# Performance work log

Measured on AMD Instinct MI355X. Metric: run time of the kernel, lower is better.

The kernel has to match this reference:

```python
import jax, jax.numpy as jnp
import numpy as np

B, S, H, E, F, TOP_K = 4, 2048, 512, 16, 1024, 2


def setup_inputs() -> dict:
    key = jax.random.key(0)
    k0, k1, k2, k3, k4 = jax.random.split(key, 5)
    scale = 0.02
    return {
        "inputs": jax.random.normal(k0, (B, S, H), dtype=jnp.float32),
        "router_w": jax.random.normal(k1, (E, H), dtype=jnp.float32) * scale,
        "gate_w": jax.random.normal(k2, (E, H, F), dtype=jnp.float32) * scale,
        "up_w": jax.random.normal(k3, (E, H, F), dtype=jnp.float32) * scale,
        "down_w": jax.random.normal(k4, (E, F, H), dtype=jnp.float32) * scale,
    }


def _moe_forward(inputs, router_w, gate_w, up_w, down_w):
    b, s, h = inputs.shape
    x = inputs.reshape(-1, h)                      # [T, H]
    T = x.shape[0]
    # --- routing: topk of logits then fp32 softmax over the k selected ---
    router_logits = x @ router_w.T                 # [T, E]
    top_vals, top_idx = jax.lax.top_k(router_logits, TOP_K)   # [T, K]
    weights = jax.nn.softmax(top_vals.astype(jnp.float32), axis=-1)  # [T, K]
    # dense combine weights: w[t, e] = routing weight if expert e selected else 0
    combine = jnp.zeros((T, router_w.shape[0]), jnp.float32)
    combine = combine.at[jnp.arange(T)[:, None], top_idx].set(weights)  # [T, E]

    # --- per-expert SwiGLU MLP, weighted combine (scan over experts) ---
    def step(acc, ew):
        wg, wu, wd, ce = ew                        # [H,F], [H,F], [F,H], [T]
        hid = jax.nn.silu(x @ wg) * (x @ wu)       # [T, F]
        y = hid @ wd                               # [T, H]
        return acc + ce[:, None] * y, None

    out0 = jnp.zeros_like(x)
    out, _ = jax.lax.scan(step, out0, (gate_w, up_w, down_w, combine.T))
    return out.reshape(b, s, h), router_logits, top_idx


def reference(inputs, router_w, gate_w, up_w, down_w):
    out, router_logits, selected_experts = _moe_forward(
        inputs, router_w, gate_w, up_w, down_w)
    return out
```

## Files before the change

kernel.cpp:

```cpp
#include <hip/hip_runtime.h>
#include <cstdint>
#include <cstddef>

#define T_TOK 8192
#define H_DIM 512
#define E_NUM 16
#define F_DIM 1024

typedef __bf16 bf16x8 __attribute__((ext_vector_type(8)));
typedef float f32x4 __attribute__((ext_vector_type(4)));

#define OFF_XBF  0UL
#define OFF_HID  8388608UL
#define OFF_GW   41943040UL
#define OFF_UW   58720256UL
#define OFF_DW   75497472UL
#define OFF_STOK 92274688UL
#define OFF_SW   92340224UL
#define OFF_TOPE 92405760UL
#define OFF_TOPW 92471296UL
#define OFF_CNT  92536832UL
#define OFF_CUR  92537856UL
#define OFF_OFFS 92538880UL

__device__ __forceinline__ unsigned short f2bf(float f) {
  union { float f; uint32_t u; } v; v.f = f;
  uint32_t r = v.u + 0x7fffu + ((v.u >> 16) & 1u);
  return (unsigned short)(r >> 16);
}

__device__ __forceinline__ void gld16(const void* g, void* l) {
  __builtin_amdgcn_global_load_lds(
      (const __attribute__((address_space(1))) unsigned int*)g,
      (__attribute__((address_space(3))) unsigned int*)l, 16, 0, 0);
}

__global__ __launch_bounds__(256) void k_pre(
    const float* __restrict__ x, const float* __restrict__ rw,
    const float* __restrict__ gw, const float* __restrict__ uw,
    const float* __restrict__ dw,
    unsigned short* __restrict__ xbf, int* __restrict__ tope,
    float* __restrict__ topw,
    unsigned short* __restrict__ gws, unsigned short* __restrict__ uws,
    unsigned short* __restrict__ dws) {
  const int bid = blockIdx.x;
  const int tid = threadIdx.x;
  __shared__ float ls[32 * 260];

  if (bid < 4096) {
    const int fx = bid & 7, kc = (bid >> 3) & 15, ez = bid >> 7;
    const int e = ez >> 1;
    const float* src = ((ez & 1) ? uw : gw) + (size_t)e * H_DIM * F_DIM;
    unsigned short* dst = ((ez & 1) ? uws : gws);
    #pragma unroll
    for (int j = 0; j < 4; ++j) {
      int vi = tid + j * 256;
      int row = vi >> 5, c4 = (vi & 31) * 4;
      float4 v = *(const float4*)&src[(size_t)(kc*32 + row) * F_DIM + fx*128 + c4];
      ls[row*132 + c4+0]=v.x; ls[row*132 + c4+1]=v.y;
      ls[row*132 + c4+2]=v.z; ls[row*132 + c4+3]=v.w;
    }
    __syncthreads();
    size_t obase = (((size_t)e * 8 + fx) * 16 + kc) * 4096;
    #pragma unroll
    for (int j = 0; j < 2; ++j) {
      int oi = tid + j * 256;
      int f = oi >> 2, slot = oi & 3;
      int ks = ((slot ^ f) & 3) * 8;
      uint4 o;
      o.x = (uint32_t)f2bf(ls[(ks+0)*132 + f]) | ((uint32_t)f2bf(ls[(ks+1)*132 + f]) << 16);
      o.y = (uint32_t)f2bf(ls[(ks+2)*132 + f]) | ((uint32_t)f2bf(ls[(ks+3)*132 + f]) << 16);
      o.z = (uint32_t)f2bf(ls[(ks+4)*132 + f]) | ((uint32_t)f2bf(ls[(ks+5)*132 + f]) << 16);
      o.w = (uint32_t)f2bf(ls[(ks+6)*132 + f]) | ((uint32_t)f2bf(ls[(ks+7)*132 + f]) << 16);
      *(uint4*)&dst[obase + (size_t)oi * 8] = o;
    }
  } else if (bid < 5120) {
    const int i = bid - 4096;
    const int ht = i & 1, kc = (i >> 1) & 31, e = i >> 6;
    const float* src = dw + (size_t)e * F_DIM * H_DIM;
    #pragma unroll
    for (int j = 0; j < 8; ++j) {
      int vi = tid + j * 256;
      int row = vi >> 6, c4 = (vi & 63) * 4;
      float4 v = *(const float4*)&src[(size_t)(kc*32 + row) * H_DIM + ht*256 + c4];
      ls[row*260 + c4+0]=v.x; ls[row*260 + c4+1]=v.y;
      ls[row*260 + c4+2]=v.z; ls[row*260 + c4+3]=v.w;
    }
    __syncthreads();
    size_t obase = (((size_t)e * 2 + ht) * 32 + kc) * 8192;
    #pragma unroll
    for (int j = 0; j < 4; ++j) {
      int oi = tid + j * 256;
      int h = oi >> 2, slot = oi & 3;
      int ks = ((slot ^ h) & 3) * 8;
      uint4 o;
      o.x = (uint32_t)f2bf(ls[(ks+0)*260 + h]) | ((uint32_t)f2bf(ls[(ks+1)*260 + h]) << 16);
      o.y = (uint32_t)f2bf(ls[(ks+2)*260 + h]) | ((uint32_t)f2bf(ls[(ks+3)*260 + h]) << 16);
      o.z = (uint32_t)f2bf(ls[(ks+4)*260 + h]) | ((uint32_t)f2bf(ls[(ks+5)*260 + h]) << 16);
      o.w = (uint32_t)f2bf(ls[(ks+6)*260 + h]) | ((uint32_t)f2bf(ls[(ks+7)*260 + h]) << 16);
      *(uint4*)&dws[obase + (size_t)oi * 8] = o;
    }
  } else {
    const int rb = bid - 5120;
    const int wave = tid >> 6, lane = tid & 63;
    const int t = rb * 4 + wave;
    const float4* xr = (const float4*)(x + (size_t)t * H_DIM + lane * 8);
    float4 a = xr[0], b = xr[1];
    float xi[8] = {a.x, a.y, a.z, a.w, b.x, b.y, b.z, b.w};
    uint4 o;
    o.x = (uint32_t)f2bf(xi[0]) | ((uint32_t)f2bf(xi[1]) << 16);
    o.y = (uint32_t)f2bf(xi[2]) | ((uint32_t)f2bf(xi[3]) << 16);
    o.z = (uint32_t)f2bf(xi[4]) | ((uint32_t)f2bf(xi[5]) << 16);
    o.w = (uint32_t)f2bf(xi[6]) | ((uint32_t)f2bf(xi[7]) << 16);
    *(uint4*)(xbf + (size_t)t * H_DIM + lane * 8) = o;
    float acc[E_NUM];
    #pragma unroll
    for (int e = 0; e < E_NUM; ++e) {
      const float4* wr = (const float4*)(rw + e * H_DIM + lane * 8);
      float4 wa = wr[0], wb = wr[1];
      acc[e] = xi[0]*wa.x + xi[1]*wa.y + xi[2]*wa.z + xi[3]*wa.w
             + xi[4]*wb.x + xi[5]*wb.y + xi[6]*wb.z + xi[7]*wb.w;
    }
    #pragma unroll
    for (int off = 1; off < 64; off <<= 1) {
      #pragma unroll
      for (int e = 0; e < E_NUM; ++e) acc[e] += __shfl_xor(acc[e], off);
    }
    if (lane == 0) {
      int e0 = 0; float v0 = acc[0];
      #pragma unroll
      for (int e = 1; e < E_NUM; ++e) if (acc[e] > v0) { v0 = acc[e]; e0 = e; }
      int e1 = -1; float v1 = -3.4e38f;
      #pragma unroll
      for (int e = 0; e < E_NUM; ++e) if (e != e0 && acc[e] > v1) { v1 = acc[e]; e1 = e; }
      float ee = __expf(v1 - v0);
      float inv = 1.0f / (1.0f + ee);
      tope[t*2]   = e0; tope[t*2+1] = e1;
      topw[t*2]   = inv; topw[t*2+1] = ee * inv;
    }
  }
}

__global__ __launch_bounds__(256) void k_hist(
    const int* __restrict__ tope, int* __restrict__ counts) {
  __shared__ int lh[E_NUM];
  const int tid = threadIdx.x;
  if (tid < E_NUM) lh[tid] = 0;
  __syncthreads();
  atomicAdd(&lh[tope[blockIdx.x * 256 + tid]], 1);
  __syncthreads();
  if (tid < E_NUM) atomicAdd(&counts[tid * 16], lh[tid]);
}

__global__ void k_offsets(const int* __restrict__ counts, int* __restrict__ offs) {
  if (threadIdx.x == 0 && blockIdx.x == 0) {
    int s = 0;
    for (int e = 0; e < E_NUM; ++e) { offs[e] = s; s += counts[e * 16]; }
    offs[E_NUM] = s;
  }
}

__global__ __launch_bounds__(256) void k_scatter(
    const int* __restrict__ tope, const float* __restrict__ topw,
    const int* __restrict__ offs, int* __restrict__ cursors,
    int* __restrict__ stok, float* __restrict__ sw) {
  __shared__ int lh[E_NUM];
  __shared__ int lbase[E_NUM];
  const int tid = threadIdx.x;
  const int t = blockIdx.x * 256 + tid;
  if (tid < E_NUM) lh[tid] = 0;
  __syncthreads();
  int e0 = tope[t*2], e1 = tope[t*2+1];
  int r0 = atomicAdd(&lh[e0], 1);
  int r1 = atomicAdd(&lh[e1], 1);
  __syncthreads();
  if (tid < E_NUM) lbase[tid] = atomicAdd(&cursors[tid * 16], lh[tid]);
  __syncthreads();
  int s0 = offs[e0] + lbase[e0] + r0;
  int s1 = offs[e1] + lbase[e1] + r1;
  stok[s0] = t; sw[s0] = topw[t*2];
  stok[s1] = t; sw[s1] = topw[t*2+1];
}

__global__ __launch_bounds__(256, 2) void k_gateup(
    const unsigned short* __restrict__ xbf,
    const unsigned short* __restrict__ gws, const unsigned short* __restrict__ uws,
    const int* __restrict__ stok, const int* __restrict__ counts,
    const int* __restrict__ offs, unsigned short* __restrict__ hid) {
  const int e = blockIdx.z;
  const int cnt = counts[e * 16];
  const int t0 = blockIdx.y * 128;
  if (t0 >= cnt) return;
  const int base = offs[e];
  const int fx = blockIdx.x;

  __shared__ __align__(16) unsigned short sb[2][3][4096];

  const int tid = threadIdx.x;
  const int wave = tid >> 6, lane = tid & 63;
  const int l15 = lane & 15, hi = lane >> 4;
  const int wm = wave >> 1, wn = wave & 1;

  const int r0 = tid >> 2, slot = tid & 3;
  const int rr0 = min(t0 + r0, cnt - 1), rr1 = min(t0 + r0 + 64, cnt - 1);
  const char* sA0 = (const char*)xbf + (size_t)stok[base + rr0] * 1024 + ((slot ^ (r0 & 3)) * 16);
  const char* sA1 = (const char*)xbf + (size_t)stok[base + rr1] * 1024 + ((slot ^ (r0 & 3)) * 16);
  const char* sG = (const char*)gws + (((size_t)e * 8 + fx) * 16) * 8192 + tid * 16;
  const char* sU = (const char*)uws + (((size_t)e * 8 + fx) * 16) * 8192 + tid * 16;
  unsigned short* const dA = &sb[0][0][wave * 512];
  unsigned short* const dG = &sb[0][1][wave * 512];
  unsigned short* const dU = &sb[0][2][wave * 512];
  const int bufo = 3 * 4096;

  f32x4 accg[4][4] = {}; f32x4 accu[4][4] = {};

  #define STAGE_GU(b, kk) { \
    gld16(sA0 + (kk)*64, dA + (b)*bufo); \
    gld16(sA1 + (kk)*64, dA + (b)*bufo + 2048); \
    gld16(sG + (size_t)(kk)*8192, dG + (b)*bufo); \
    gld16(sG + (size_t)(kk)*8192 + 4096, dG + (b)*bufo + 2048); \
    gld16(sU + (size_t)(kk)*8192, dU + (b)*bufo); \
    gld16(sU + (size_t)(kk)*8192 + 4096, dU + (b)*bufo + 2048); }

  STAGE_GU(0, 0);
  __syncthreads();
  #pragma unroll 1
  for (int kk = 0; kk < 16; ++kk) {
    const int cur = kk & 1;
    if (kk < 15) STAGE_GU(cur ^ 1, kk + 1);
    const unsigned short* lA = &sb[cur][0][0];
    const unsigned short* lG = &sb[cur][1][0];
    const unsigned short* lU = &sb[cur][2][0];
    bf16x8 a[4], bg[4], bu[4];
    #pragma unroll
    for (int m = 0; m < 4; ++m) {
      int row = wm*64 + m*16 + l15;
      a[m] = *(const bf16x8*)((const char*)lA + row*64 + (((hi ^ row) & 3) << 4));
    }
    #pragma unroll
    for (int s = 0; s < 4; ++s) {
      int row = wn*64 + s*16 + l15;
      int o = row*64 + (((hi ^ row) & 3) << 4);
      bg[s] = *(const bf16x8*)((const char*)lG + o);
      bu[s] = *(const bf16x8*)((const char*)lU + o);
    }
    #pragma unroll
    for (int m = 0; m < 4; ++m)
      #pragma unroll
      for (int s = 0; s < 4; ++s) {
        accg[m][s] = __builtin_amdgcn_mfma_f32_16x16x32_bf16(a[m], bg[s], accg[m][s], 0, 0, 0);
        accu[m][s] = __builtin_amdgcn_mfma_f32_16x16x32_bf16(a[m], bu[s], accu[m][s], 0, 0, 0);
      }
    __syncthreads();
  }
  #undef STAGE_GU

  #pragma unroll
  for (int m = 0; m < 4; ++m)
    #pragma unroll
    for (int r = 0; r < 4; ++r) {
      int row = t0 + wm*64 + m*16 + hi*4 + r;
      if (row < cnt) {
        #pragma unroll
        for (int s = 0; s < 4; ++s) {
          float g = accg[m][s][r], u = accu[m][s][r];
          float h = g / (1.0f + __expf(-g)) * u;
          hid[(size_t)(base + row) * 1024 + fx*128 + wn*64 + s*16 + l15] = f2bf(h);
        }
      }
    }
}

__global__ __launch_bounds__(256, 3) void k_down(
    const unsigned short* __restrict__ hid, const unsigned short* __restrict__ dws,
    const int* __restrict__ stok, const float* __restrict__ sw,
    const int* __restrict__ counts, const int* __restrict__ offs,
    float* __restrict__ out) {
  const int e = blockIdx.z;
  const int cnt = counts[e * 16];
  const int t0 = blockIdx.y * 64;
  if (t0 >= cnt) return;
  const int base = offs[e];
  const int ht = blockIdx.x;

  __shared__ __align__(16) unsigned short sbA[2][2048];
  __shared__ __align__(16) unsigned short sbW[2][8192];

  const int tid = threadIdx.x;
  const int wave = tid >> 6, lane = tid & 63;
  const int l15 = lane & 15, hi = lane >> 4;

  const int r0 = tid >> 2, slot = tid & 3;
  const int rr = min(t0 + r0, cnt - 1);
  const char* sA = (const char*)hid + (size_t)(base + rr) * 2048 + ((slot ^ (r0 & 3)) * 16);
  const char* sW = (const char*)dws + (((size_t)e * 2 + ht) * 32) * 16384 + tid * 16;
  unsigned short* const dA = &sbA[0][wave * 512];
  unsigned short* const dW = &sbW[0][wave * 512];

  f32x4 acc[4][4] = {};

  #define STAGE_DN(b, kk) { \
    gld16(sA + (kk)*64, dA + (b)*2048); \
    const char* w = sW + (size_t)(kk)*16384; \
    gld16(w,         dW + (b)*8192); \
    gld16(w + 4096,  dW + (b)*8192 + 2048); \
    gld16(w + 8192,  dW + (b)*8192 + 4096); \
    gld16(w + 12288, dW + (b)*8192 + 6144); }

  STAGE_DN(0, 0);
  __syncthreads();
  #pragma unroll 1
  for (int kk = 0; kk < 32; ++kk) {
    const int cur = kk & 1;
    if (kk < 31) STAGE_DN(cur ^ 1, kk + 1);
    const unsigned short* lA = &sbA[cur][0];
    const unsigned short* lW = &sbW[cur][0];
    bf16x8 a[4], b[4];
    #pragma unroll
    for (int m = 0; m < 4; ++m) {
      int row = m*16 + l15;
      a[m] = *(const bf16x8*)((const char*)lA + row*64 + (((hi ^ row) & 3) << 4));
    }
    #pragma unroll
    for (int s = 0; s < 4; ++s) {
      int row = wave*64 + s*16 + l15;
      b[s] = *(const bf16x8*)((const char*)lW + row*64 + (((hi ^ row) & 3) << 4));
    }
    #pragma unroll
    for (int m = 0; m < 4; ++m)
      #pragma unroll
      for (int s = 0; s < 4; ++s)
        acc[m][s] = __builtin_amdgcn_mfma_f32_16x16x32_bf16(a[m], b[s], acc[m][s], 0, 0, 0);
    __syncthreads();
  }
  #undef STAGE_DN

  #pragma unroll
  for (int m = 0; m < 4; ++m)
    #pragma unroll
    for (int r = 0; r < 4; ++r) {
      int row = t0 + m*16 + hi*4 + r;
      if (row < cnt) {
        int sl = base + row;
        int t = stok[sl];
        float w = sw[sl];
        float* orow = out + (size_t)t * H_DIM + ht*256 + wave*64;
        #pragma unroll
        for (int s = 0; s < 4; ++s)
          atomicAdd(&orow[s*16 + l15], w * acc[m][s][r]);
      }
    }
}

extern "C" void kernel_launch(void* const* d_in, const int* in_sizes, int n_in,
                              void* d_out, int out_size, void* d_ws, size_t ws_size,
                              hipStream_t stream) {
  const float* x  = (const float*)d_in[0];
  const float* rw = (const float*)d_in[1];
  const float* gw = (const float*)d_in[2];
  const float* uw = (const float*)d_in[3];
  const float* dw = (const float*)d_in[4];
  float* out = (float*)d_out;
  char* ws = (char*)d_ws;

  unsigned short* xbf = (unsigned short*)(ws + OFF_XBF);
  unsigned short* hid = (unsigned short*)(ws + OFF_HID);
  unsigned short* gws = (unsigned short*)(ws + OFF_GW);
  unsigned short* uws = (unsigned short*)(ws + OFF_UW);
  unsigned short* dws = (unsigned short*)(ws + OFF_DW);
  int*   stok    = (int*)(ws + OFF_STOK);
  float* swt     = (float*)(ws + OFF_SW);
  int*   tope    = (int*)(ws + OFF_TOPE);
  float* topw    = (float*)(ws + OFF_TOPW);
  int*   counts  = (int*)(ws + OFF_CNT);
  int*   cursors = (int*)(ws + OFF_CUR);
  int*   offs    = (int*)(ws + OFF_OFFS);

  hipMemsetAsync(ws + OFF_CNT, 0, 2048 + 128, stream);
  hipMemsetAsync(d_out, 0, (size_t)T_TOK * H_DIM * sizeof(float), stream);

  k_pre<<<7168, 256, 0, stream>>>(x, rw, gw, uw, dw, xbf, tope, topw, gws, uws, dws);
  k_hist<<<T_TOK * 2 / 256, 256, 0, stream>>>(tope, counts);
  k_offsets<<<1, 64, 0, stream>>>(counts, offs);
  k_scatter<<<T_TOK / 256, 256, 0, stream>>>(tope, topw, offs, cursors, stok, swt);
  k_gateup<<<dim3(8, T_TOK * 2 / 128, E_NUM), 256, 0, stream>>>(
      xbf, gws, uws, stok, counts, offs, hid);
  k_down<<<dim3(2, T_TOK * 2 / 64, E_NUM), 256, 0, stream>>>(
      hid, dws, stok, swt, counts, offs, out);
}
```

Before: 172.9 us.

## Replace atomic scatter-add combine with bf16 expert outputs and per-token gather

The down-projection kernel now writes unweighted bf16 results per sorted slot into a buffer that reuses the gate-weight workspace region, instead of doing weighted fp32 atomicAdds into the output. A new gather kernel reads each token's two slot rows via a recorded slot index, applies the routing weights and writes the output once. This removes the output memset and the contended atomics, at the cost of an extra kernel launch, an intermediate buffer round trip, and bf16 rounding of expert outputs before combining.

Measured after the change: 158.1 us. 1.09x faster.

```diff
diff --git a/kernel.cpp b/kernel.cpp
--- a/kernel.cpp
+++ b/kernel.cpp
@@ -22,11 +22,18 @@
 #define OFF_CNT  92536832UL
 #define OFF_CUR  92537856UL
 #define OFF_OFFS 92538880UL
+#define OFF_SIDX 92539904UL
+#define OFF_YB   OFF_GW
 
 __device__ __forceinline__ unsigned short f2bf(float f) {
   union { float f; uint32_t u; } v; v.f = f;
   uint32_t r = v.u + 0x7fffu + ((v.u >> 16) & 1u);
   return (unsigned short)(r >> 16);
+}
+
+__device__ __forceinline__ float bf2f(unsigned short u) {
+  union { uint32_t u; float f; } v; v.u = (uint32_t)u << 16;
+  return v.f;
 }
 
 __device__ __forceinline__ void gld16(const void* g, void* l) {
@@ -163,7 +170,7 @@
 __global__ __launch_bounds__(256) void k_scatter(
     const int* __restrict__ tope, const float* __restrict__ topw,
     const int* __restrict__ offs, int* __restrict__ cursors,
-    int* __restrict__ stok, float* __restrict__ sw) {
+    int* __restrict__ stok, float* __restrict__ sw, int* __restrict__ sidx) {
   __shared__ int lh[E_NUM];
   __shared__ int lbase[E_NUM];
   const int tid = threadIdx.x;
@@ -180,6 +187,7 @@
   int s1 = offs[e1] + lbase[e1] + r1;
   stok[s0] = t; sw[s0] = topw[t*2];
   stok[s1] = t; sw[s1] = topw[t*2+1];
+  sidx[t*2] = s0; sidx[t*2+1] = s1;
 }
 
 __global__ __launch_bounds__(256, 2) void k_gateup(
@@ -273,9 +281,8 @@
 
 __global__ __launch_bounds__(256, 3) void k_down(
     const unsigned short* __restrict__ hid, const unsigned short* __restrict__ dws,
-    const int* __restrict__ stok, const float* __restrict__ sw,
     const int* __restrict__ counts, const int* __restrict__ offs,
-    float* __restrict__ out) {
+    unsigned short* __restrict__ ybuf) {
   const int e = blockIdx.z;
   const int cnt = counts[e * 16];
   const int t0 = blockIdx.y * 64;
@@ -341,15 +348,35 @@
     for (int r = 0; r < 4; ++r) {
       int row = t0 + m*16 + hi*4 + r;
       if (row < cnt) {
-        int sl = base + row;
-        int t = stok[sl];
-        float w = sw[sl];
-        float* orow = out + (size_t)t * H_DIM + ht*256 + wave*64;
+        unsigned short* y = ybuf + (size_t)(base + row) * 512 + ht*256 + wave*64;
         #pragma unroll
         for (int s = 0; s < 4; ++s)
-          atomicAdd(&orow[s*16 + l15], w * acc[m][s][r]);
+          y[s*16 + l15] = f2bf(acc[m][s][r]);
       }
     }
+}
+
+__global__ __launch_bounds__(256) void k_gather(
+    const unsigned short* __restrict__ ybuf, const int* __restrict__ sidx,
+    const float* __restrict__ topw, float* __restrict__ out) {
+  const int wave = threadIdx.x >> 6, lane = threadIdx.x & 63;
+  const int t = blockIdx.x * 4 + wave;
+  const int s0 = sidx[t*2], s1 = sidx[t*2+1];
+  const float w0 = topw[t*2], w1 = topw[t*2+1];
+  uint4 a = *(const uint4*)(ybuf + (size_t)s0 * 512 + lane * 8);
+  uint4 b = *(const uint4*)(ybuf + (size_t)s1 * 512 + lane * 8);
+  float4 o0, o1;
+  o0.x = w0*bf2f((unsigned short)(a.x)) + w1*bf2f((unsigned short)(b.x));
+  o0.y = w0*bf2f((unsigned short)(a.x>>16)) + w1*bf2f((unsigned short)(b.x>>16));
+  o0.z = w0*bf2f((unsigned short)(a.y)) + w1*bf2f((unsigned short)(b.y));
+  o0.w = w0*bf2f((unsigned short)(a.y>>16)) + w1*bf2f((unsigned short)(b.y>>16));
+  o1.x = w0*bf2f((unsigned short)(a.z)) + w1*bf2f((unsigned short)(b.z));
+  o1.y = w0*bf2f((unsigned short)(a.z>>16)) + w1*bf2f((unsigned short)(b.z>>16));
+  o1.z = w0*bf2f((unsigned short)(a.w)) + w1*bf2f((unsigned short)(b.w));
+  o1.w = w0*bf2f((unsigned short)(a.w>>16)) + w1*bf2f((unsigned short)(b.w>>16));
+  float* orow = out + (size_t)t * H_DIM + lane * 8;
+  *(float4*)orow = o0;
+  *(float4*)(orow + 4) = o1;
 }
 
 extern "C" void kernel_launch(void* const* d_in, const int* in_sizes, int n_in,
@@ -368,6 +395,7 @@
   unsigned short* gws = (unsigned short*)(ws + OFF_GW);
   unsigned short* uws = (unsigned short*)(ws + OFF_UW);
   unsigned short* dws = (unsigned short*)(ws + OFF_DW);
+  unsigned short* ybuf = (unsigned short*)(ws + OFF_YB);
   int*   stok    = (int*)(ws + OFF_STOK);
   float* swt     = (float*)(ws + OFF_SW);
   int*   tope    = (int*)(ws + OFF_TOPE);
@@ -375,16 +403,17 @@
   int*   counts  = (int*)(ws + OFF_CNT);
   int*   cursors = (int*)(ws + OFF_CUR);
   int*   offs    = (int*)(ws + OFF_OFFS);
+  int*   sidx    = (int*)(ws + OFF_SIDX);
 
   hipMemsetAsync(ws + OFF_CNT, 0, 2048 + 128, stream);
-  hipMemsetAsync(d_out, 0, (size_t)T_TOK * H_DIM * sizeof(float), stream);
 
   k_pre<<<7168, 256, 0, stream>>>(x, rw, gw, uw, dw, xbf, tope, topw, gws, uws, dws);
   k_hist<<<T_TOK * 2 / 256, 256, 0, stream>>>(tope, counts);
   k_offsets<<<1, 64, 0, stream>>>(counts, offs);
-  k_scatter<<<T_TOK / 256, 256, 0, stream>>>(tope, topw, offs, cursors, stok, swt);
+  k_scatter<<<T_TOK / 256, 256, 0, stream>>>(tope, topw, offs, cursors, stok, swt, sidx);
   k_gateup<<<dim3(8, T_TOK * 2 / 128, E_NUM), 256, 0, stream>>>(
       xbf, gws, uws, stok, counts, offs, hid);
   k_down<<<dim3(2, T_TOK * 2 / 64, E_NUM), 256, 0, stream>>>(
-      hid, dws, stok, swt, counts, offs, out);
-}
+      hid, dws, counts, offs, ybuf);
+  k_gather<<<T_TOK / 4, 256, 0, stream>>>(ybuf, sidx, topw, out);
+}
```
